# Kernel optimization log

Hardware: AMD Instinct MI355X
Metric: run time of the kernel (lower is better)

Reference implementation:

```python
import jax, jax.numpy as jnp
import numpy as np

NEG = -1000000000.0

def setup_inputs() -> dict:
    key = jax.random.key(0)
    k1, k2, k3, k4 = jax.random.split(key, 4)
    B, T, D, V = 64, 512, 768, 20
    embeddings = jax.random.normal(k1, (B, T, D), dtype=jnp.float32)
    embeddings_mask = jax.random.randint(k2, (B, T), 0, 2, dtype=jnp.int32)
    value_mask = jax.random.randint(k3, (B, V), 0, 2, dtype=jnp.int32)
    value_weight = jax.random.normal(k4, (V, D), dtype=jnp.float32)
    return {"embeddings": embeddings, "embeddings_mask": embeddings_mask,
            "value_mask": value_mask, "value_weight": value_weight}

def reference(embeddings, embeddings_mask, value_mask, value_weight):
    # value attention: scores[b,t,v] = <emb[b,t], W[v]>  (torch does bcast-mul-sum)
    emb_mask = embeddings_mask.astype(jnp.float32)          # (B,T)
    scores = jnp.einsum('btd,vd->btv', embeddings, value_weight)
    scores = scores * emb_mask[:, :, None]                   # mask tokens
    value_scores = scores.sum(axis=1)                        # (B,V)
    value_scores = value_scores + (1.0 - value_mask.astype(jnp.float32)) * NEG
    value_probs = jax.nn.softmax(value_scores, axis=-1)      # (B,V)
    value_embedding = jnp.einsum('bv,vd->bd', value_probs, value_weight)
    # attention pooling over tokens using value_embedding as query
    pooling_scores = jnp.einsum('btd,bd->bt', embeddings, value_embedding)
    pooling_scores = pooling_scores + (1.0 - emb_mask) * NEG
    pooling_probs = jax.nn.softmax(pooling_scores, axis=-1)  # (B,T)
    pooled_embedding = jnp.einsum('btd,bt->bd', embeddings, pooling_probs)
    return (value_embedding, pooled_embedding, value_probs, pooling_probs)
```

## Files before the change

### kernel.cpp

```cpp
#include <hip/hip_runtime.h>
#include <math.h>

#define B 64
#define T 512
#define D 768
#define D4 (D / 4)
#define V 20
#define NEG -1000000000.0f
#define TCH 32
#define NCH (T / TCH)

__global__ __launch_bounds__(192) void k_masked_sum(
    const float4* __restrict__ emb4, const int* __restrict__ emask,
    float4* __restrict__ part4) {
  int b = blockIdx.x / NCH;
  int c = blockIdx.x % NCH;
  int tid = threadIdx.x;
  __shared__ int sm[TCH];
  if (tid < TCH) sm[tid] = emask[b * T + c * TCH + tid];
  __syncthreads();
  float4 a = {0.f, 0.f, 0.f, 0.f};
  const float4* eb = emb4 + ((size_t)b * T + (size_t)c * TCH) * D4 + tid;
  for (int tt = 0; tt < TCH; ++tt) {
    if (sm[tt]) {
      float4 e = eb[(size_t)tt * D4];
      a.x += e.x; a.y += e.y; a.z += e.z; a.w += e.w;
    }
  }
  part4[(size_t)blockIdx.x * D4 + tid] = a;
}

__global__ __launch_bounds__(256) void k_value(
    const float* __restrict__ part, const int* __restrict__ vmask,
    const float* __restrict__ W, float* __restrict__ out_vemb,
    float* __restrict__ out_vprobs) {
  int b = blockIdx.x;
  int tid = threadIdx.x;
  __shared__ float msum[D];
  __shared__ float sc[V];
  __shared__ float pr[V];
  for (int k = 0; k < 3; ++k) {
    int d = tid + 256 * k;
    float s = 0.f;
    for (int c = 0; c < NCH; ++c) s += part[((size_t)(b * NCH + c)) * D + d];
    msum[d] = s;
  }
  __syncthreads();
  int wave = tid >> 6, lane = tid & 63;
  for (int v = wave; v < V; v += 4) {
    float p = 0.f;
    for (int j = 0; j < 12; ++j) {
      int d = lane + 64 * j;
      p += msum[d] * W[(size_t)v * D + d];
    }
    for (int off = 32; off; off >>= 1) p += __shfl_down(p, off, 64);
    if (lane == 0) sc[v] = p + (vmask[b * V + v] ? 0.f : NEG);
  }
  __syncthreads();
  if (tid == 0) {
    float m = sc[0];
    for (int v = 1; v < V; ++v) m = fmaxf(m, sc[v]);
    float s = 0.f;
    for (int v = 0; v < V; ++v) {
      float e = expf(sc[v] - m);
      pr[v] = e;
      s += e;
    }
    float inv = 1.f / s;
    for (int v = 0; v < V; ++v) {
      pr[v] *= inv;
      out_vprobs[b * V + v] = pr[v];
    }
  }
  __syncthreads();
  for (int k = 0; k < 3; ++k) {
    int d = tid + 256 * k;
    float a = 0.f;
    for (int v = 0; v < V; ++v) a += pr[v] * W[(size_t)v * D + d];
    out_vemb[(size_t)b * D + d] = a;
  }
}

__global__ __launch_bounds__(256) void k_fused_pool(
    const float4* __restrict__ emb4, const int* __restrict__ emask,
    const float4* __restrict__ vemb4, float* __restrict__ scores,
    float* __restrict__ pm, float* __restrict__ pl,
    float4* __restrict__ pacc4) {
  int b = blockIdx.x / NCH;
  int c = blockIdx.x % NCH;
  int tid = threadIdx.x;
  int wave = tid >> 6, lane = tid & 63;
  __shared__ int sm[TCH];
  __shared__ float lm[4], ll[4];
  __shared__ float lacc[4][D];
  if (tid < TCH) sm[tid] = emask[b * T + c * TCH + tid];
  __syncthreads();

  float4 ve[3];
  for (int j = 0; j < 3; ++j) ve[j] = vemb4[(size_t)b * D4 + lane + 64 * j];

  float m = NEG, l = 0.f;
  float4 acc[3];
  for (int j = 0; j < 3; ++j) acc[j] = {0.f, 0.f, 0.f, 0.f};

  const float4* eb = emb4 + ((size_t)b * T + (size_t)c * TCH) * D4;
  for (int tt = wave; tt < TCH; tt += 4) {
    if (!sm[tt]) {
      if (lane == 0) scores[b * T + c * TCH + tt] = NEG;
      continue;
    }
    float4 e[3];
    for (int j = 0; j < 3; ++j) e[j] = eb[(size_t)tt * D4 + lane + 64 * j];
    float p = 0.f;
    for (int j = 0; j < 3; ++j)
      p += e[j].x * ve[j].x + e[j].y * ve[j].y + e[j].z * ve[j].z +
           e[j].w * ve[j].w;
    for (int off = 32; off; off >>= 1) p += __shfl_xor(p, off, 64);
    if (lane == 0) scores[b * T + c * TCH + tt] = p;
    if (p > m) {
      float scale = expf(m - p);
      l *= scale;
      for (int j = 0; j < 3; ++j) {
        acc[j].x *= scale; acc[j].y *= scale;
        acc[j].z *= scale; acc[j].w *= scale;
      }
      m = p;
    }
    float w = expf(p - m);
    l += w;
    for (int j = 0; j < 3; ++j) {
      acc[j].x += w * e[j].x; acc[j].y += w * e[j].y;
      acc[j].z += w * e[j].z; acc[j].w += w * e[j].w;
    }
  }

  if (lane == 0) { lm[wave] = m; ll[wave] = l; }
  for (int j = 0; j < 3; ++j)
    *(float4*)&lacc[wave][4 * (lane + 64 * j)] = acc[j];
  __syncthreads();

  __shared__ float co[4];
  __shared__ float sM, sL;
  if (tid == 0) {
    float M = fmaxf(fmaxf(lm[0], lm[1]), fmaxf(lm[2], lm[3]));
    float L = 0.f;
    for (int w2 = 0; w2 < 4; ++w2) {
      co[w2] = expf(lm[w2] - M);
      L += ll[w2] * co[w2];
    }
    sM = M; sL = L;
    pm[blockIdx.x] = M;
    pl[blockIdx.x] = L;
  }
  __syncthreads();
  if (tid < D4) {
    float4 s = {0.f, 0.f, 0.f, 0.f};
    for (int w2 = 0; w2 < 4; ++w2) {
      float cw = co[w2];
      float4 a = *(float4*)&lacc[w2][4 * tid];
      s.x += cw * a.x; s.y += cw * a.y; s.z += cw * a.z; s.w += cw * a.w;
    }
    pacc4[(size_t)blockIdx.x * D4 + tid] = s;
  }
}

__global__ __launch_bounds__(256) void k_pool_final(
    const float* __restrict__ pm, const float* __restrict__ pl,
    const float* __restrict__ pacc, const float* __restrict__ scores,
    const int* __restrict__ emask, float* __restrict__ pooled,
    float* __restrict__ pprobs) {
  int b = blockIdx.x, tid = threadIdx.x;
  __shared__ float co[NCH];
  __shared__ float sM, sinvL;
  if (tid == 0) {
    float M = NEG;
    for (int c = 0; c < NCH; ++c) M = fmaxf(M, pm[b * NCH + c]);
    float L = 0.f;
    for (int c = 0; c < NCH; ++c) L += pl[b * NCH + c] * expf(pm[b * NCH + c] - M);
    float invL = 1.f / L;
    for (int c = 0; c < NCH; ++c) co[c] = expf(pm[b * NCH + c] - M) * invL;
    sM = M; sinvL = invL;
  }
  __syncthreads();
  for (int k = 0; k < 3; ++k) {
    int d = tid + 256 * k;
    float s = 0.f;
    for (int c = 0; c < NCH; ++c) s += pacc[((size_t)(b * NCH + c)) * D + d] * co[c];
    pooled[(size_t)b * D + d] = s;
  }
  for (int k = 0; k < 2; ++k) {
    int t = tid + 256 * k;
    pprobs[b * T + t] =
        emask[b * T + t] ? expf(scores[b * T + t] - sM) * sinvL : 0.f;
  }
}

extern "C" void kernel_launch(void* const* d_in, const int* in_sizes, int n_in,
                              void* d_out, int out_size, void* d_ws,
                              size_t ws_size, hipStream_t stream) {
  const float* emb = (const float*)d_in[0];
  const int* emask = (const int*)d_in[1];
  const int* vmask = (const int*)d_in[2];
  const float* W = (const float*)d_in[3];

  float* out = (float*)d_out;
  float* vemb_out = out;
  float* pooled_out = out + B * D;
  float* vprobs_out = out + 2 * B * D;
  float* pprobs_out = out + 2 * B * D + B * V;

  float* ws = (float*)d_ws;
  float* part = ws;
  float* scores = ws + B * NCH * D;
  float* pm = scores + B * T;
  float* pl = pm + B * NCH;

  k_masked_sum<<<B * NCH, 192, 0, stream>>>((const float4*)emb, emask,
                                            (float4*)part);
  k_value<<<B, 256, 0, stream>>>(part, vmask, W, vemb_out, vprobs_out);
  k_fused_pool<<<B * NCH, 256, 0, stream>>>((const float4*)emb, emask,
                                            (const float4*)vemb_out, scores, pm,
                                            pl, (float4*)part);
  k_pool_final<<<B, 256, 0, stream>>>(pm, pl, part, scores, emask, pooled_out,
                                      pprobs_out);
}
```

Before: 171.7 us.

## Fuse all stages into one persistent kernel with software grid barriers

Replaces the four separate kernel launches with a single kernel of 512 blocks that synchronises through atomic-counter grid barriers. Each block keeps its chunk's compacted list of unmasked token indices in shared memory, and chunks grow from 32 to 64 tokens. Each chunk's partial value scores are reduced per block before the first barrier, so full masked sums never go through global memory. Loops are unrolled two tokens at a time, with a merged online-softmax update. The design relies on all 512 blocks being co-resident to avoid deadlock, adds a memset launch, and spins on atomics; the second embedding pass may now hit cache because it runs right after the first.

```diff
diff --git a/kernel.cpp b/kernel.cpp
--- a/kernel.cpp
+++ b/kernel.cpp
@@ -4,201 +4,278 @@
 #define B 64
 #define T 512
 #define D 768
-#define D4 (D / 4)
+#define D4 192
 #define V 20
 #define NEG -1000000000.0f
-#define TCH 32
-#define NCH (T / TCH)
-
-__global__ __launch_bounds__(192) void k_masked_sum(
+#define TCH 64
+#define NCH 8
+#define NBLK 512
+#define NTHR 256
+
+__device__ __forceinline__ void grid_barrier(unsigned* cnt) {
+  __syncthreads();
+  if (threadIdx.x == 0) {
+    __threadfence();
+    atomicAdd(cnt, 1u);
+    while (atomicAdd(cnt, 0u) < (unsigned)NBLK) __builtin_amdgcn_s_sleep(1);
+    __threadfence();
+  }
+  __syncthreads();
+}
+
+__global__ __launch_bounds__(NTHR, 2) void k_fused_all(
     const float4* __restrict__ emb4, const int* __restrict__ emask,
-    float4* __restrict__ part4) {
-  int b = blockIdx.x / NCH;
-  int c = blockIdx.x % NCH;
-  int tid = threadIdx.x;
-  __shared__ int sm[TCH];
-  if (tid < TCH) sm[tid] = emask[b * T + c * TCH + tid];
+    const int* __restrict__ vmask, const float* __restrict__ W,
+    float* __restrict__ vemb_out, float* __restrict__ pooled_out,
+    float* __restrict__ vprobs_out, float* __restrict__ pprobs_out,
+    float* __restrict__ ws, unsigned* __restrict__ bar) {
+  const int bc = blockIdx.x;
+  const int b = bc >> 3;
+  const int c = bc & 7;
+  const int tid = threadIdx.x;
+  const int wave = tid >> 6, lane = tid & 63;
+
+  float* pacc = ws;
+  float* scores = pacc + NBLK * D;
+  float* pm = scores + B * T;
+  float* pl = pm + NBLK;
+  float* pd = pl + NBLK;
+
+  __shared__ float4 lacc4[4][D4];
+  __shared__ float msum[D];
+  __shared__ int idx[TCH];
+  __shared__ int scnt;
+  __shared__ float lm[4], ll[4], coS[NCH];
+  __shared__ float sc[V], pr[V];
+  __shared__ float sM, sinvL;
+
+  if (tid == 0) {
+    int n = 0;
+    const int* em = emask + b * T + c * TCH;
+    for (int t = 0; t < TCH; ++t)
+      if (em[t]) idx[n++] = t;
+    scnt = n;
+  }
   __syncthreads();
-  float4 a = {0.f, 0.f, 0.f, 0.f};
-  const float4* eb = emb4 + ((size_t)b * T + (size_t)c * TCH) * D4 + tid;
-  for (int tt = 0; tt < TCH; ++tt) {
-    if (sm[tt]) {
-      float4 e = eb[(size_t)tt * D4];
-      a.x += e.x; a.y += e.y; a.z += e.z; a.w += e.w;
-    }
-  }
-  part4[(size_t)blockIdx.x * D4 + tid] = a;
-}
-
-__global__ __launch_bounds__(256) void k_value(
-    const float* __restrict__ part, const int* __restrict__ vmask,
-    const float* __restrict__ W, float* __restrict__ out_vemb,
-    float* __restrict__ out_vprobs) {
-  int b = blockIdx.x;
-  int tid = threadIdx.x;
-  __shared__ float msum[D];
-  __shared__ float sc[V];
-  __shared__ float pr[V];
-  for (int k = 0; k < 3; ++k) {
-    int d = tid + 256 * k;
-    float s = 0.f;
-    for (int c = 0; c < NCH; ++c) s += part[((size_t)(b * NCH + c)) * D + d];
-    msum[d] = s;
-  }
-  __syncthreads();
-  int wave = tid >> 6, lane = tid & 63;
-  for (int v = wave; v < V; v += 4) {
-    float p = 0.f;
-    for (int j = 0; j < 12; ++j) {
-      int d = lane + 64 * j;
-      p += msum[d] * W[(size_t)v * D + d];
-    }
-    for (int off = 32; off; off >>= 1) p += __shfl_down(p, off, 64);
-    if (lane == 0) sc[v] = p + (vmask[b * V + v] ? 0.f : NEG);
-  }
-  __syncthreads();
-  if (tid == 0) {
-    float m = sc[0];
-    for (int v = 1; v < V; ++v) m = fmaxf(m, sc[v]);
-    float s = 0.f;
-    for (int v = 0; v < V; ++v) {
-      float e = expf(sc[v] - m);
-      pr[v] = e;
-      s += e;
-    }
-    float inv = 1.f / s;
-    for (int v = 0; v < V; ++v) {
-      pr[v] *= inv;
-      out_vprobs[b * V + v] = pr[v];
-    }
-  }
-  __syncthreads();
-  for (int k = 0; k < 3; ++k) {
-    int d = tid + 256 * k;
-    float a = 0.f;
-    for (int v = 0; v < V; ++v) a += pr[v] * W[(size_t)v * D + d];
-    out_vemb[(size_t)b * D + d] = a;
-  }
-}
-
-__global__ __launch_bounds__(256) void k_fused_pool(
-    const float4* __restrict__ emb4, const int* __restrict__ emask,
-    const float4* __restrict__ vemb4, float* __restrict__ scores,
-    float* __restrict__ pm, float* __restrict__ pl,
-    float4* __restrict__ pacc4) {
-  int b = blockIdx.x / NCH;
-  int c = blockIdx.x % NCH;
-  int tid = threadIdx.x;
-  int wave = tid >> 6, lane = tid & 63;
-  __shared__ int sm[TCH];
-  __shared__ float lm[4], ll[4];
-  __shared__ float lacc[4][D];
-  if (tid < TCH) sm[tid] = emask[b * T + c * TCH + tid];
-  __syncthreads();
-
-  float4 ve[3];
-  for (int j = 0; j < 3; ++j) ve[j] = vemb4[(size_t)b * D4 + lane + 64 * j];
-
-  float m = NEG, l = 0.f;
-  float4 acc[3];
-  for (int j = 0; j < 3; ++j) acc[j] = {0.f, 0.f, 0.f, 0.f};
-
+  const int cnt = scnt;
   const float4* eb = emb4 + ((size_t)b * T + (size_t)c * TCH) * D4;
-  for (int tt = wave; tt < TCH; tt += 4) {
-    if (!sm[tt]) {
-      if (lane == 0) scores[b * T + c * TCH + tt] = NEG;
-      continue;
-    }
-    float4 e[3];
-    for (int j = 0; j < 3; ++j) e[j] = eb[(size_t)tt * D4 + lane + 64 * j];
-    float p = 0.f;
-    for (int j = 0; j < 3; ++j)
-      p += e[j].x * ve[j].x + e[j].y * ve[j].y + e[j].z * ve[j].z +
-           e[j].w * ve[j].w;
-    for (int off = 32; off; off >>= 1) p += __shfl_xor(p, off, 64);
-    if (lane == 0) scores[b * T + c * TCH + tt] = p;
-    if (p > m) {
-      float scale = expf(m - p);
-      l *= scale;
-      for (int j = 0; j < 3; ++j) {
-        acc[j].x *= scale; acc[j].y *= scale;
-        acc[j].z *= scale; acc[j].w *= scale;
-      }
-      m = p;
-    }
-    float w = expf(p - m);
-    l += w;
-    for (int j = 0; j < 3; ++j) {
-      acc[j].x += w * e[j].x; acc[j].y += w * e[j].y;
-      acc[j].z += w * e[j].z; acc[j].w += w * e[j].w;
-    }
-  }
-
-  if (lane == 0) { lm[wave] = m; ll[wave] = l; }
-  for (int j = 0; j < 3; ++j)
-    *(float4*)&lacc[wave][4 * (lane + 64 * j)] = acc[j];
-  __syncthreads();
-
-  __shared__ float co[4];
-  __shared__ float sM, sL;
-  if (tid == 0) {
-    float M = fmaxf(fmaxf(lm[0], lm[1]), fmaxf(lm[2], lm[3]));
-    float L = 0.f;
-    for (int w2 = 0; w2 < 4; ++w2) {
-      co[w2] = expf(lm[w2] - M);
-      L += ll[w2] * co[w2];
-    }
-    sM = M; sL = L;
-    pm[blockIdx.x] = M;
-    pl[blockIdx.x] = L;
-  }
-  __syncthreads();
-  if (tid < D4) {
-    float4 s = {0.f, 0.f, 0.f, 0.f};
-    for (int w2 = 0; w2 < 4; ++w2) {
-      float cw = co[w2];
-      float4 a = *(float4*)&lacc[w2][4 * tid];
-      s.x += cw * a.x; s.y += cw * a.y; s.z += cw * a.z; s.w += cw * a.w;
-    }
-    pacc4[(size_t)blockIdx.x * D4 + tid] = s;
-  }
-}
-
-__global__ __launch_bounds__(256) void k_pool_final(
-    const float* __restrict__ pm, const float* __restrict__ pl,
-    const float* __restrict__ pacc, const float* __restrict__ scores,
-    const int* __restrict__ emask, float* __restrict__ pooled,
-    float* __restrict__ pprobs) {
-  int b = blockIdx.x, tid = threadIdx.x;
-  __shared__ float co[NCH];
-  __shared__ float sM, sinvL;
-  if (tid == 0) {
-    float M = NEG;
-    for (int c = 0; c < NCH; ++c) M = fmaxf(M, pm[b * NCH + c]);
-    float L = 0.f;
-    for (int c = 0; c < NCH; ++c) L += pl[b * NCH + c] * expf(pm[b * NCH + c] - M);
-    float invL = 1.f / L;
-    for (int c = 0; c < NCH; ++c) co[c] = expf(pm[b * NCH + c] - M) * invL;
-    sM = M; sinvL = invL;
-  }
-  __syncthreads();
-  for (int k = 0; k < 3; ++k) {
-    int d = tid + 256 * k;
-    float s = 0.f;
-    for (int c = 0; c < NCH; ++c) s += pacc[((size_t)(b * NCH + c)) * D + d] * co[c];
-    pooled[(size_t)b * D + d] = s;
-  }
-  for (int k = 0; k < 2; ++k) {
-    int t = tid + 256 * k;
-    pprobs[b * T + t] =
-        emask[b * T + t] ? expf(scores[b * T + t] - sM) * sinvL : 0.f;
+
+  {
+    float4 s0 = {0.f, 0.f, 0.f, 0.f}, s1 = s0, s2 = s0;
+    int i = wave;
+    for (; i + 4 < cnt; i += 8) {
+      const float4* ea = eb + (size_t)idx[i] * D4 + lane;
+      const float4* ec = eb + (size_t)idx[i + 4] * D4 + lane;
+      float4 a0 = ea[0], a1 = ea[64], a2 = ea[128];
+      float4 b0 = ec[0], b1 = ec[64], b2 = ec[128];
+      s0.x += a0.x + b0.x; s0.y += a0.y + b0.y;
+      s0.z += a0.z + b0.z; s0.w += a0.w + b0.w;
+      s1.x += a1.x + b1.x; s1.y += a1.y + b1.y;
+      s1.z += a1.z + b1.z; s1.w += a1.w + b1.w;
+      s2.x += a2.x + b2.x; s2.y += a2.y + b2.y;
+      s2.z += a2.z + b2.z; s2.w += a2.w + b2.w;
+    }
+    if (i < cnt) {
+      const float4* ea = eb + (size_t)idx[i] * D4 + lane;
+      float4 a0 = ea[0], a1 = ea[64], a2 = ea[128];
+      s0.x += a0.x; s0.y += a0.y; s0.z += a0.z; s0.w += a0.w;
+      s1.x += a1.x; s1.y += a1.y; s1.z += a1.z; s1.w += a1.w;
+      s2.x += a2.x; s2.y += a2.y; s2.z += a2.z; s2.w += a2.w;
+    }
+    lacc4[wave][lane] = s0;
+    lacc4[wave][lane + 64] = s1;
+    lacc4[wave][lane + 128] = s2;
+    __syncthreads();
+    if (tid < D4) {
+      float4 a = lacc4[0][tid], x = lacc4[1][tid], y = lacc4[2][tid],
+             z = lacc4[3][tid];
+      float4 r;
+      r.x = a.x + x.x + y.x + z.x;
+      r.y = a.y + x.y + y.y + z.y;
+      r.z = a.z + x.z + y.z + z.z;
+      r.w = a.w + x.w + y.w + z.w;
+      *(float4*)&msum[4 * tid] = r;
+    }
+    __syncthreads();
+    for (int v = wave; v < V; v += 4) {
+      float p = 0.f;
+      const float* wv = W + (size_t)v * D;
+      for (int j = 0; j < 12; ++j) {
+        int d = lane + 64 * j;
+        p += msum[d] * wv[d];
+      }
+      for (int off = 32; off; off >>= 1) p += __shfl_xor(p, off, 64);
+      if (lane == 0) pd[bc * V + v] = p;
+    }
+  }
+  grid_barrier(bar + 0);
+
+  if (bc < B) {
+    if (tid < V) {
+      float s = 0.f;
+      for (int cc = 0; cc < NCH; ++cc) s += pd[(bc * NCH + cc) * V + tid];
+      sc[tid] = s + (vmask[bc * V + tid] ? 0.f : NEG);
+    }
+    __syncthreads();
+    if (tid == 0) {
+      float m = sc[0];
+      for (int v = 1; v < V; ++v) m = fmaxf(m, sc[v]);
+      float ssum = 0.f;
+      for (int v = 0; v < V; ++v) {
+        float e = expf(sc[v] - m);
+        pr[v] = e;
+        ssum += e;
+      }
+      float inv = 1.f / ssum;
+      for (int v = 0; v < V; ++v) {
+        pr[v] *= inv;
+        vprobs_out[bc * V + v] = pr[v];
+      }
+    }
+    __syncthreads();
+    if (tid < D4) {
+      float4 a = {0.f, 0.f, 0.f, 0.f};
+      for (int v = 0; v < V; ++v) {
+        float p = pr[v];
+        float4 w4 = *(const float4*)&W[(size_t)v * D + 4 * tid];
+        a.x += p * w4.x; a.y += p * w4.y;
+        a.z += p * w4.z; a.w += p * w4.w;
+      }
+      ((float4*)vemb_out)[(size_t)bc * D4 + tid] = a;
+    }
+  }
+  grid_barrier(bar + 1);
+
+  {
+    const float4* vb = (const float4*)vemb_out + (size_t)b * D4;
+    float4 ve0 = vb[lane], ve1 = vb[lane + 64], ve2 = vb[lane + 128];
+    float* srow = scores + b * T + c * TCH;
+    float m = NEG, l = 0.f;
+    float4 a0 = {0.f, 0.f, 0.f, 0.f}, a1 = a0, a2 = a0;
+    int i = wave;
+    for (; i + 4 < cnt; i += 8) {
+      int t0 = idx[i], t1 = idx[i + 4];
+      const float4* ea = eb + (size_t)t0 * D4 + lane;
+      const float4* ec = eb + (size_t)t1 * D4 + lane;
+      float4 e0 = ea[0], e1 = ea[64], e2 = ea[128];
+      float4 f0 = ec[0], f1 = ec[64], f2 = ec[128];
+      float p0 = e0.x * ve0.x + e0.y * ve0.y + e0.z * ve0.z + e0.w * ve0.w +
+                 e1.x * ve1.x + e1.y * ve1.y + e1.z * ve1.z + e1.w * ve1.w +
+                 e2.x * ve2.x + e2.y * ve2.y + e2.z * ve2.z + e2.w * ve2.w;
+      float p1 = f0.x * ve0.x + f0.y * ve0.y + f0.z * ve0.z + f0.w * ve0.w +
+                 f1.x * ve1.x + f1.y * ve1.y + f1.z * ve1.z + f1.w * ve1.w +
+                 f2.x * ve2.x + f2.y * ve2.y + f2.z * ve2.z + f2.w * ve2.w;
+      for (int off = 32; off; off >>= 1) {
+        p0 += __shfl_xor(p0, off, 64);
+        p1 += __shfl_xor(p1, off, 64);
+      }
+      if (lane == 0) { srow[t0] = p0; srow[t1] = p1; }
+      float mn = fmaxf(m, fmaxf(p0, p1));
+      float scale = expf(m - mn);
+      float w0 = expf(p0 - mn), w1 = expf(p1 - mn);
+      l = l * scale + w0 + w1;
+      a0.x = a0.x * scale + w0 * e0.x + w1 * f0.x;
+      a0.y = a0.y * scale + w0 * e0.y + w1 * f0.y;
+      a0.z = a0.z * scale + w0 * e0.z + w1 * f0.z;
+      a0.w = a0.w * scale + w0 * e0.w + w1 * f0.w;
+      a1.x = a1.x * scale + w0 * e1.x + w1 * f1.x;
+      a1.y = a1.y * scale + w0 * e1.y + w1 * f1.y;
+      a1.z = a1.z * scale + w0 * e1.z + w1 * f1.z;
+      a1.w = a1.w * scale + w0 * e1.w + w1 * f1.w;
+      a2.x = a2.x * scale + w0 * e2.x + w1 * f2.x;
+      a2.y = a2.y * scale + w0 * e2.y + w1 * f2.y;
+      a2.z = a2.z * scale + w0 * e2.z + w1 * f2.z;
+      a2.w = a2.w * scale + w0 * e2.w + w1 * f2.w;
+      m = mn;
+    }
+    if (i < cnt) {
+      int t0 = idx[i];
+      const float4* ea = eb + (size_t)t0 * D4 + lane;
+      float4 e0 = ea[0], e1 = ea[64], e2 = ea[128];
+      float p0 = e0.x * ve0.x + e0.y * ve0.y + e0.z * ve0.z + e0.w * ve0.w +
+                 e1.x * ve1.x + e1.y * ve1.y + e1.z * ve1.z + e1.w * ve1.w +
+                 e2.x * ve2.x + e2.y * ve2.y + e2.z * ve2.z + e2.w * ve2.w;
+      for (int off = 32; off; off >>= 1) p0 += __shfl_xor(p0, off, 64);
+      if (lane == 0) srow[t0] = p0;
+      float mn = fmaxf(m, p0);
+      float scale = expf(m - mn);
+      float w0 = expf(p0 - mn);
+      l = l * scale + w0;
+      a0.x = a0.x * scale + w0 * e0.x; a0.y = a0.y * scale + w0 * e0.y;
+      a0.z = a0.z * scale + w0 * e0.z; a0.w = a0.w * scale + w0 * e0.w;
+      a1.x = a1.x * scale + w0 * e1.x; a1.y = a1.y * scale + w0 * e1.y;
+      a1.z = a1.z * scale + w0 * e1.z; a1.w = a1.w * scale + w0 * e1.w;
+      a2.x = a2.x * scale + w0 * e2.x; a2.y = a2.y * scale + w0 * e2.y;
+      a2.z = a2.z * scale + w0 * e2.z; a2.w = a2.w * scale + w0 * e2.w;
+      m = mn;
+    }
+    if (lane == 0) { lm[wave] = m; ll[wave] = l; }
+    lacc4[wave][lane] = a0;
+    lacc4[wave][lane + 64] = a1;
+    lacc4[wave][lane + 128] = a2;
+    __syncthreads();
+    if (tid == 0) {
+      float M = fmaxf(fmaxf(lm[0], lm[1]), fmaxf(lm[2], lm[3]));
+      float L = 0.f;
+      for (int w2 = 0; w2 < 4; ++w2) {
+        float cw = expf(lm[w2] - M);
+        coS[w2] = cw;
+        L += ll[w2] * cw;
+      }
+      pm[bc] = M;
+      pl[bc] = L;
+    }
+    __syncthreads();
+    if (tid < D4) {
+      float4 r = {0.f, 0.f, 0.f, 0.f};
+      for (int w2 = 0; w2 < 4; ++w2) {
+        float cw = coS[w2];
+        float4 a = lacc4[w2][tid];
+        r.x += cw * a.x; r.y += cw * a.y;
+        r.z += cw * a.z; r.w += cw * a.w;
+      }
+      ((float4*)pacc)[(size_t)bc * D4 + tid] = r;
+    }
+  }
+  grid_barrier(bar + 2);
+
+  if (bc < B) {
+    if (tid == 0) {
+      float M = NEG;
+      for (int cc = 0; cc < NCH; ++cc) M = fmaxf(M, pm[bc * NCH + cc]);
+      float L = 0.f;
+      for (int cc = 0; cc < NCH; ++cc)
+        L += pl[bc * NCH + cc] * expf(pm[bc * NCH + cc] - M);
+      float invL = 1.f / L;
+      for (int cc = 0; cc < NCH; ++cc)
+        coS[cc] = expf(pm[bc * NCH + cc] - M) * invL;
+      sM = M;
+      sinvL = invL;
+    }
+    __syncthreads();
+    if (tid < D4) {
+      float4 r = {0.f, 0.f, 0.f, 0.f};
+      for (int cc = 0; cc < NCH; ++cc) {
+        float cw = coS[cc];
+        float4 a = ((const float4*)pacc)[(size_t)(bc * NCH + cc) * D4 + tid];
+        r.x += cw * a.x; r.y += cw * a.y;
+        r.z += cw * a.z; r.w += cw * a.w;
+      }
+      ((float4*)pooled_out)[(size_t)bc * D4 + tid] = r;
+    }
+    float M = sM, invL = sinvL;
+    for (int k = 0; k < 2; ++k) {
+      int t = tid + 256 * k;
+      pprobs_out[bc * T + t] =
+          emask[bc * T + t] ? expf(scores[bc * T + t] - M) * invL : 0.f;
+    }
   }
 }
 
 extern "C" void kernel_launch(void* const* d_in, const int* in_sizes, int n_in,
                               void* d_out, int out_size, void* d_ws,
                               size_t ws_size, hipStream_t stream) {
-  const float* emb = (const float*)d_in[0];
+  const float4* emb4 = (const float4*)d_in[0];
   const int* emask = (const int*)d_in[1];
   const int* vmask = (const int*)d_in[2];
   const float* W = (const float*)d_in[3];
@@ -210,17 +287,11 @@
   float* pprobs_out = out + 2 * B * D + B * V;
 
   float* ws = (float*)d_ws;
-  float* part = ws;
-  float* scores = ws + B * NCH * D;
-  float* pm = scores + B * T;
-  float* pl = pm + B * NCH;
-
-  k_masked_sum<<<B * NCH, 192, 0, stream>>>((const float4*)emb, emask,
-                                            (float4*)part);
-  k_value<<<B, 256, 0, stream>>>(part, vmask, W, vemb_out, vprobs_out);
-  k_fused_pool<<<B * NCH, 256, 0, stream>>>((const float4*)emb, emask,
-                                            (const float4*)vemb_out, scores, pm,
-                                            pl, (float4*)part);
-  k_pool_final<<<B, 256, 0, stream>>>(pm, pl, part, scores, emask, pooled_out,
-                                      pprobs_out);
+  size_t ws_floats = (size_t)NBLK * D + B * T + 2 * NBLK + NBLK * V;
+  unsigned* bar = (unsigned*)(ws + ws_floats);
+
+  hipMemsetAsync(bar, 0, 64, stream);
+  k_fused_all<<<dim3(NBLK), dim3(NTHR), 0, stream>>>(
+      emb4, emask, vmask, W, vemb_out, pooled_out, vprobs_out, pprobs_out, ws,
+      bar);
 }
```

Measured after the change: 298.7 us. 73.9% more time.
